# Kernel tuning notes

Measured on AMD Instinct MI355X. Metric: run time of the kernel, lower is better.

The kernel has to match this reference:

```python
import jax, jax.numpy as jnp
import numpy as np

N_NODES = 50000
N_EDGES = 800000
N_GRAPHS = 128
D_IN, D_HID, D_OUT = 128, 128, 128  # gnn_input_dim, gnn_hidden_dim, gnn_output_dim
EPS = 1e-5
NEG_SLOPE = 0.01


def setup_inputs() -> dict:
    key = jax.random.key(0)
    ks = jax.random.split(key, 16)
    x = jax.random.normal(ks[0], (N_NODES, D_IN), jnp.float32)
    edge_index = jax.random.randint(ks[1], (2, N_EDGES), 0, N_NODES, dtype=jnp.int64)
    batch = jnp.sort(jax.random.randint(ks[2], (N_NODES,), 0, N_GRAPHS, dtype=jnp.int64))

    def lin(k, fi, fo):
        return jax.random.normal(k, (fi, fo), jnp.float32) * (1.0 / np.sqrt(fi))

    d2, d4 = 2 * D_HID, 4 * D_HID
    return {
        "x": x, "edge_index": edge_index, "batch": batch, "batch_size": N_GRAPHS,
        "W1": lin(ks[3], D_IN, d2), "b1": jnp.zeros((d2,), jnp.float32),
        "g1": jnp.ones((d2,), jnp.float32), "be1": jnp.zeros((d2,), jnp.float32),
        "W2": lin(ks[4], d2, d4), "b2": jnp.zeros((d4,), jnp.float32),
        "g2": jnp.ones((d4,), jnp.float32), "be2": jnp.zeros((d4,), jnp.float32),
        "W3": lin(ks[5], d4, d4), "b3": jnp.zeros((d4,), jnp.float32),
        "g3": jnp.ones((d4,), jnp.float32), "be3": jnp.zeros((d4,), jnp.float32),
        "Wf": lin(ks[6], d4, D_OUT), "bf": jnp.zeros((D_OUT,), jnp.float32),
    }


def _layernorm(h, g, b):
    mu = jnp.mean(h, axis=-1, keepdims=True)
    var = jnp.mean(jnp.square(h - mu), axis=-1, keepdims=True)
    return (h - mu) * jax.lax.rsqrt(var + EPS) * g + b


def _gcn_conv(h, W, b, src, dst, norm, n):
    # h' = D^-1/2 (A+I) D^-1/2 (h W) + b   (PyG GCNConv with self-loops)
    m = h @ W                                    # [N, F_out]
    msg = m[src] * norm[:, None]                 # [E+N, F_out]
    return jax.ops.segment_sum(msg, dst, num_segments=n) + b


def reference(x, edge_index, batch, batch_size, W1, b1, g1, be1,
              W2, b2, g2, be2, W3, b3, g3, be3, Wf, bf):
    n = x.shape[0]
    loop = jnp.arange(n, dtype=edge_index.dtype)
    src = jnp.concatenate([edge_index[0], loop])
    dst = jnp.concatenate([edge_index[1], loop])
    deg = jax.ops.segment_sum(jnp.ones_like(dst, dtype=x.dtype), dst, num_segments=n)
    dinv = jax.lax.rsqrt(deg)                    # deg >= 1 due to self loops
    norm = dinv[src] * dinv[dst]

    h = _gcn_conv(x, W1, b1, src, dst, norm, n)
    h = jax.nn.leaky_relu(_layernorm(h, g1, be1), NEG_SLOPE)
    h = _gcn_conv(h, W2, b2, src, dst, norm, n)
    h = jax.nn.leaky_relu(_layernorm(h, g2, be2), NEG_SLOPE)
    h = _gcn_conv(h, W3, b3, src, dst, norm, n)
    h = _layernorm(h, g3, be3)

    # global average pool per graph
    sums = jax.ops.segment_sum(h, batch, num_segments=batch_size)
    cnt = jax.ops.segment_sum(jnp.ones((n,), h.dtype), batch, num_segments=batch_size)
    pooled = sums / jnp.maximum(cnt, 1.0)[:, None]
    return pooled @ Wf + bf
```

## Files before the change

### kernel.cpp

```cpp
#include <hip/hip_runtime.h>
#include <hip/hip_bf16.h>
#include <math.h>

#define GRAPHS 128
#define SCAN_B 256
#define BM 128
#define BN 128
#define PCH 128

typedef __attribute__((ext_vector_type(4))) int i32x4;

__device__ inline unsigned short f2b(float f) {
    unsigned int u = __float_as_uint(f);
    unsigned int r = (u + 0x7fffu + ((u >> 16) & 1u)) >> 16;
    return (unsigned short)r;
}
__device__ inline float b2f(unsigned short u) {
    return __uint_as_float(((unsigned int)u) << 16);
}
__device__ inline void unpack8(float* v, uint4 u) {
    v[0] = b2f(u.x & 0xffffu); v[1] = b2f(u.x >> 16);
    v[2] = b2f(u.y & 0xffffu); v[3] = b2f(u.y >> 16);
    v[4] = b2f(u.z & 0xffffu); v[5] = b2f(u.z >> 16);
    v[6] = b2f(u.w & 0xffffu); v[7] = b2f(u.w >> 16);
}

__device__ inline void gload16(const void* g, void* l) {
    typedef unsigned int __attribute__((address_space(1))) gu32;
    typedef unsigned int __attribute__((address_space(3))) su32;
    __builtin_amdgcn_global_load_lds((const gu32*)g, (su32*)l, 16, 0, 0);
}

__device__ inline int xcd_vid(int p, int nwg) {
    int q = nwg >> 3, r = nwg & 7, x = p & 7, ix = p >> 3;
    return (x < r ? x * (q + 1) : r * (q + 1) + (x - r) * q) + ix;
}


__global__ void k_count(const int* __restrict__ dst, int* __restrict__ cnt, int E) {
    int i = blockIdx.x * blockDim.x + threadIdx.x;
    if (i < E) atomicAdd(&cnt[dst[i]], 1);
}

__global__ void k_scan1(const int* __restrict__ cnt, int* __restrict__ excl,
                        int* __restrict__ bsum, int n) {
    __shared__ int sh[SCAN_B];
    int t = threadIdx.x;
    int i = blockIdx.x * SCAN_B + t;
    int v = (i < n) ? cnt[i] : 0;
    sh[t] = v;
    __syncthreads();
    for (int off = 1; off < SCAN_B; off <<= 1) {
        int x = (t >= off) ? sh[t - off] : 0;
        __syncthreads();
        sh[t] += x;
        __syncthreads();
    }
    if (i < n) excl[i] = sh[t] - v;
    if (t == SCAN_B - 1) bsum[blockIdx.x] = sh[t];
}

__global__ void k_scan2(int* __restrict__ bsum, int nb) {
    __shared__ int sh[SCAN_B];
    int t = threadIdx.x;
    int v = (t < nb) ? bsum[t] : 0;
    sh[t] = v;
    __syncthreads();
    for (int off = 1; off < SCAN_B; off <<= 1) {
        int x = (t >= off) ? sh[t - off] : 0;
        __syncthreads();
        sh[t] += x;
        __syncthreads();
    }
    if (t < nb) bsum[t] = sh[t] - v;
}

__global__ void k_scan3(int* __restrict__ rowstart, const int* __restrict__ bsum,
                        const int* __restrict__ cnt, float* __restrict__ dinv,
                        int* __restrict__ cursor, int n, int E) {
    int i = blockIdx.x * SCAN_B + threadIdx.x;
    if (i < n) {
        rowstart[i] += bsum[blockIdx.x];
        cursor[i] = 0;
        dinv[i] = rsqrtf((float)cnt[i] + 1.0f);
    }
    if (i == 0) rowstart[n] = E;
}

__global__ void k_scatter_csr(const int* __restrict__ src, const int* __restrict__ dst,
                              const float* __restrict__ dinv, const int* __restrict__ rowstart,
                              int* __restrict__ cursor, int2* __restrict__ csr, int E) {
    int e = blockIdx.x * blockDim.x + threadIdx.x;
    if (e >= E) return;
    int s = src[e], d = dst[e];
    int pos = rowstart[d] + atomicAdd(&cursor[d], 1);
    int2 c;
    c.x = s;
    c.y = __float_as_int(dinv[s] * dinv[d]);
    csr[pos] = c;
}


__global__ void k_wtq(const float* __restrict__ W1, const float* __restrict__ W2,
                      const float* __restrict__ W3, signed char* __restrict__ T1,
                      signed char* __restrict__ T2, signed char* __restrict__ T3,
                      float* __restrict__ S1, float* __restrict__ S2,
                      float* __restrict__ S3) {
    int w = blockIdx.x * 4 + (threadIdx.x >> 6);
    int lane = threadIdx.x & 63;
    const float* W; signed char* T; float* S; int K, N, col;
    if (w < 256) { W = W1; T = T1; S = S1; K = 128; N = 256; col = w; }
    else if (w < 768) { W = W2; T = T2; S = S2; K = 256; N = 512; col = w - 256; }
    else { W = W3; T = T3; S = S3; K = 512; N = 512; col = w - 768; }
    int epl = K >> 6;
    float v[8];
    float mx = 0.f;
    for (int j = 0; j < epl; ++j) {
        float x = W[(size_t)(lane * epl + j) * N + col];
        v[j] = x;
        mx = fmaxf(mx, fabsf(x));
    }
#pragma unroll
    for (int m = 1; m < 64; m <<= 1) mx = fmaxf(mx, __shfl_xor(mx, m));
    float inv = (mx > 0.f) ? 127.0f / mx : 0.f;
    signed char* tp = T + (size_t)col * K + lane * epl;
    for (int j = 0; j < epl; ++j) tp[j] = (signed char)__float2int_rn(v[j] * inv);
    if (lane == 0) S[col] = mx * (1.0f / 127.0f);
}


__global__ void k_x2q(const float* __restrict__ x, signed char* __restrict__ q,
                      float* __restrict__ sc, int n, int mpad) {
    int row = blockIdx.x * 4 + (threadIdx.x >> 6);
    int lane = threadIdx.x & 63;
    if (row >= mpad) return;
    signed char* qp = q + (size_t)row * 128 + lane * 2;
    if (row >= n) {
        *(unsigned short*)qp = 0;
        if (lane == 0) sc[row] = 0.f;
        return;
    }
    float2 v = *(const float2*)(x + (size_t)row * 128 + lane * 2);
    float mx = fmaxf(fabsf(v.x), fabsf(v.y));
#pragma unroll
    for (int m = 1; m < 64; m <<= 1) mx = fmaxf(mx, __shfl_xor(mx, m));
    float inv = (mx > 0.f) ? 127.0f / mx : 0.f;
    int q0 = __float2int_rn(v.x * inv), q1 = __float2int_rn(v.y * inv);
    *(unsigned short*)qp = (unsigned short)((q0 & 0xff) | ((q1 & 0xff) << 8));
    if (lane == 0) sc[row] = mx * (1.0f / 127.0f);
}


__device__ inline void acc8i(float* a, uint2 u, float w) {
    a[0] += (float)(signed char)(u.x) * w;
    a[1] += (float)(signed char)(u.x >> 8) * w;
    a[2] += (float)(signed char)(u.x >> 16) * w;
    a[3] += (float)(signed char)(u.x >> 24) * w;
    a[4] += (float)(signed char)(u.y) * w;
    a[5] += (float)(signed char)(u.y >> 8) * w;
    a[6] += (float)(signed char)(u.y >> 16) * w;
    a[7] += (float)(signed char)(u.y >> 24) * w;
}

template <int F>
__global__ void k_agg8(const signed char* __restrict__ q8, const float* __restrict__ scale,
                       signed char* __restrict__ qa, float* __restrict__ sa,
                       const int* __restrict__ rowstart, const int2* __restrict__ csr,
                       const float* __restrict__ dinv, int n, int mpad) {
    constexpr int TPN = F / 8;
    constexpr int NPB = 256 / TPN;
    int node = blockIdx.x * NPB + (int)(threadIdx.x / TPN);
    int sub = (int)(threadIdx.x % TPN);
    int fo = sub * 8;
    if (node >= mpad) return;
    signed char* outp = qa + (size_t)node * F + fo;
    if (node >= n) {
        *(uint2*)outp = uint2{0u, 0u};
        if (sub == 0) sa[node] = 0.f;
        return;
    }

    const signed char* qf = q8 + fo;
    float di = dinv[node];
    float a[8] = {};
    {
        uint2 u = *(const uint2*)(qf + (size_t)node * F);
        acc8i(a, u, di * di * scale[node]);
    }
    int b = rowstart[node], e = rowstart[node + 1];
    int j = b;
    for (; j + 2 <= e; j += 2) {
        int2 c0 = csr[j], c1 = csr[j + 1];
        uint2 u0 = *(const uint2*)(qf + (size_t)c0.x * F);
        uint2 u1 = *(const uint2*)(qf + (size_t)c1.x * F);
        float w0 = __int_as_float(c0.y) * scale[c0.x];
        float w1 = __int_as_float(c1.y) * scale[c1.x];
        acc8i(a, u0, w0);
        acc8i(a, u1, w1);
    }
    for (; j < e; ++j) {
        int2 c = csr[j];
        uint2 u = *(const uint2*)(qf + (size_t)c.x * F);
        acc8i(a, u, __int_as_float(c.y) * scale[c.x]);
    }
    float mx = 0.f;
#pragma unroll
    for (int k = 0; k < 8; ++k) mx = fmaxf(mx, fabsf(a[k]));
#pragma unroll
    for (int m = 1; m < TPN; m <<= 1) mx = fmaxf(mx, __shfl_xor(mx, m));
    float inv = (mx > 0.f) ? 127.0f / mx : 0.f;
    unsigned int o0 = 0, o1 = 0;
#pragma unroll
    for (int k = 0; k < 4; ++k) {
        o0 |= ((unsigned)(__float2int_rn(a[k] * inv) & 0xff)) << (8 * k);
        o1 |= ((unsigned)(__float2int_rn(a[k + 4] * inv) & 0xff)) << (8 * k);
    }
    *(uint2*)outp = uint2{o0, o1};
    if (sub == 0) sa[node] = mx * (1.0f / 127.0f);
}


__global__ __launch_bounds__(256) void k_gemm_i8(
    const signed char* __restrict__ A, const float* __restrict__ srow,
    const signed char* __restrict__ BT, const float* __restrict__ scol,
    const float* __restrict__ bias, unsigned short* __restrict__ C,
    int K, int N, int ncb) {
    __shared__ __align__(16) char sA[BM * 128];
    __shared__ __align__(16) char sB[BN * 128];

    const int vid = xcd_vid((int)blockIdx.x, (int)gridDim.x);
    const int rb = vid / ncb;
    const int cb = vid - rb * ncb;
    const int tid = threadIdx.x;
    const int lane = tid & 63;
    const int wave = tid >> 6;
    const int wr = wave >> 1, wc = wave & 1;
    const size_t row0 = (size_t)rb * BM;
    const size_t col0 = (size_t)cb * BN;

    const signed char* srcA[4];
    const signed char* srcB[4];
    char* dstA[4];
    char* dstB[4];
#pragma unroll
    for (int c = 0; c < 4; ++c) {
        int idx = c * 256 + tid;
        int row = idx >> 3;
        int cbl = ((idx & 7) << 4) ^ ((row & 7) << 4);
        srcA[c] = A + (row0 + row) * K + cbl;
        srcB[c] = BT + (col0 + row) * K + cbl;
        dstA[c] = sA + idx * 16;
        dstB[c] = sB + idx * 16;
    }

    const int fr = lane & 15;
    const int fg = lane >> 4;
    const int fsw = (lane & 7) << 4;
    int offA[4][2], offB[4][2];
#pragma unroll
    for (int t = 0; t < 4; ++t)
#pragma unroll
        for (int kk = 0; kk < 2; ++kk) {
            offA[t][kk] = (wr * 64 + t * 16 + fr) * 128 + ((kk * 64 + fg * 16) ^ fsw);
            offB[t][kk] = (wc * 64 + t * 16 + fr) * 128 + ((kk * 64 + fg * 16) ^ fsw);
        }

    i32x4 acc[4][4] = {};

    for (int k0 = 0; k0 < K; k0 += 128) {
#pragma unroll
        for (int c = 0; c < 4; ++c) gload16(srcA[c] + k0, dstA[c]);
#pragma unroll
        for (int c = 0; c < 4; ++c) gload16(srcB[c] + k0, dstB[c]);
        __syncthreads();
#pragma unroll
        for (int kk = 0; kk < 2; ++kk) {
            i32x4 av[4], bv[4];
#pragma unroll
            for (int t = 0; t < 4; ++t) av[t] = *(const i32x4*)(sA + offA[t][kk]);
#pragma unroll
            for (int t = 0; t < 4; ++t) bv[t] = *(const i32x4*)(sB + offB[t][kk]);
#pragma unroll
            for (int i = 0; i < 4; ++i)
#pragma unroll
                for (int j = 0; j < 4; ++j)
                    acc[i][j] = __builtin_amdgcn_mfma_i32_16x16x64_i8(av[i], bv[j],
                                                                      acc[i][j], 0, 0, 0);
        }
        __syncthreads();
    }

    float sr[4][4];
#pragma unroll
    for (int i = 0; i < 4; ++i)
#pragma unroll
        for (int q = 0; q < 4; ++q)
            sr[i][q] = srow[row0 + wr * 64 + i * 16 + fg * 4 + q];

#pragma unroll
    for (int i = 0; i < 4; ++i) {
#pragma unroll
        for (int j = 0; j < 4; ++j) {
            size_t r = row0 + wr * 64 + i * 16 + fg * 4;
            size_t cc = col0 + wc * 64 + j * 16 + fr;
            float scc = scol[cc];
            float bb = bias[cc];
#pragma unroll
            for (int q = 0; q < 4; ++q)
                C[(r + q) * N + cc] = f2b((float)acc[i][j][q] * (sr[i][q] * scc) + bb);
        }
    }
}


template <int F, bool LRELU>
__global__ void k_lnr8(const unsigned short* __restrict__ z, signed char* __restrict__ q8,
                       float* __restrict__ scale, const float* __restrict__ g,
                       const float* __restrict__ be, int mpad) {
    constexpr int V = F / 64;
    int row = blockIdx.x * 4 + (threadIdx.x >> 6);
    int lane = threadIdx.x & 63;
    const unsigned short* p = z + (size_t)row * F + lane * V;
    float v[V];
    if constexpr (V == 8) {
        uint4 u = *(const uint4*)p;
        unpack8(v, u);
    } else {
        uint2 u = *(const uint2*)p;
        v[0] = b2f(u.x & 0xffffu); v[1] = b2f(u.x >> 16);
        v[2] = b2f(u.y & 0xffffu); v[3] = b2f(u.y >> 16);
    }
    float s = 0.f, q = 0.f;
#pragma unroll
    for (int k = 0; k < V; ++k) { s += v[k]; q += v[k] * v[k]; }
#pragma unroll
    for (int m = 1; m < 64; m <<= 1) {
        s += __shfl_xor(s, m);
        q += __shfl_xor(q, m);
    }
    float mu = s * (1.0f / F);
    float var = q * (1.0f / F) - mu * mu;
    float rs = rsqrtf(var + 1e-5f);

    float y[V];
    float mx = 0.f;
#pragma unroll
    for (int k = 0; k < V; ++k) {
        float yy = (v[k] - mu) * rs * g[lane * V + k] + be[lane * V + k];
        if (LRELU) yy = fmaxf(yy, 0.f) + 0.01f * fminf(yy, 0.f);
        y[k] = yy;
        mx = fmaxf(mx, fabsf(yy));
    }
#pragma unroll
    for (int m = 1; m < 64; m <<= 1) mx = fmaxf(mx, __shfl_xor(mx, m));

    float inv = (mx > 0.f) ? 127.0f / mx : 0.f;
    unsigned int ob[V / 4];
#pragma unroll
    for (int k = 0; k < V; k += 4) {
        int q0 = __float2int_rn(y[k] * inv);
        int q1 = __float2int_rn(y[k + 1] * inv);
        int q2 = __float2int_rn(y[k + 2] * inv);
        int q3 = __float2int_rn(y[k + 3] * inv);
        ob[k / 4] = (q0 & 0xff) | ((q1 & 0xff) << 8) | ((q2 & 0xff) << 16) | ((q3 & 0xff) << 24);
    }
    signed char* qp = q8 + (size_t)row * F + lane * V;
    if constexpr (V == 8) *(uint2*)qp = *(uint2*)ob;
    else                  *(unsigned int*)qp = ob[0];
    if (lane == 0) scale[row] = mx * (1.0f / 127.0f);
}


__global__ void k_pool4(const unsigned short* __restrict__ z, const float* __restrict__ g,
                        const float* __restrict__ be, const int* __restrict__ batch,
                        float* __restrict__ pooled, int n) {
    int i0 = blockIdx.x * PCH;
    int iend = i0 + PCH; if (iend > n) iend = n;
    int w = threadIdx.x >> 6, lane = threadIdx.x & 63;
    int f0 = lane * 8;
    float gk[8], ek[8];
    {
        float4 ga = *(const float4*)(g + f0), gb = *(const float4*)(g + f0 + 4);
        float4 ea = *(const float4*)(be + f0), eb = *(const float4*)(be + f0 + 4);
        gk[0] = ga.x; gk[1] = ga.y; gk[2] = ga.z; gk[3] = ga.w;
        gk[4] = gb.x; gk[5] = gb.y; gk[6] = gb.z; gk[7] = gb.w;
        ek[0] = ea.x; ek[1] = ea.y; ek[2] = ea.z; ek[3] = ea.w;
        ek[4] = eb.x; ek[5] = eb.y; ek[6] = eb.z; ek[7] = eb.w;
    }
    float a[8] = {};
    int cur = -1;
    for (int i = i0 + w; i < iend; i += 4) {
        int gg = batch[i];
        if (gg != cur) {
            if (cur >= 0) {
                float* pp = pooled + (size_t)cur * 512 + f0;
#pragma unroll
                for (int k = 0; k < 8; ++k) atomicAdd(&pp[k], a[k]);
            }
#pragma unroll
            for (int k = 0; k < 8; ++k) a[k] = 0.f;
            cur = gg;
        }
        uint4 u = *(const uint4*)(z + (size_t)i * 512 + f0);
        float v[8]; unpack8(v, u);
        float s = 0.f, q = 0.f;
#pragma unroll
        for (int k = 0; k < 8; ++k) { s += v[k]; q += v[k] * v[k]; }
#pragma unroll
        for (int m = 1; m < 64; m <<= 1) {
            s += __shfl_xor(s, m);
            q += __shfl_xor(q, m);
        }
        float mu = s * (1.0f / 512.0f);
        float var = q * (1.0f / 512.0f) - mu * mu;
        float rs = rsqrtf(var + 1e-5f);
#pragma unroll
        for (int k = 0; k < 8; ++k) a[k] += (v[k] - mu) * rs * gk[k] + ek[k];
    }
    if (cur >= 0) {
        float* pp = pooled + (size_t)cur * 512 + f0;
#pragma unroll
        for (int k = 0; k < 8; ++k) atomicAdd(&pp[k], a[k]);
    }
}


__global__ void k_final(const float* __restrict__ pooled, const int* __restrict__ batch,
                        const float* __restrict__ Wf, const float* __restrict__ bf,
                        float* __restrict__ out, int n) {
    int gph = blockIdx.x;
    int o = threadIdx.x;
    int lo = 0, hi = n;
    while (lo < hi) { int mid = (lo + hi) >> 1; if (batch[mid] < gph) lo = mid + 1; else hi = mid; }
    int start = lo;
    lo = start; hi = n;
    while (lo < hi) { int mid = (lo + hi) >> 1; if (batch[mid] < gph + 1) lo = mid + 1; else hi = mid; }
    int end = lo;
    float inv = 1.0f / fmaxf((float)(end - start), 1.0f);

    __shared__ float p[512];
    for (int k = threadIdx.x; k < 512; k += 128) p[k] = pooled[(size_t)gph * 512 + k] * inv;
    __syncthreads();
    float acc = bf[o];
#pragma unroll 8
    for (int k = 0; k < 512; ++k) acc += p[k] * Wf[(size_t)k * 128 + o];
    out[(size_t)gph * 128 + o] = acc;
}


static inline size_t align_up(size_t x) { return (x + 255) & ~(size_t)255; }

extern "C" void kernel_launch(void* const* d_in, const int* in_sizes, int n_in,
                              void* d_out, int out_size, void* d_ws, size_t ws_size,
                              hipStream_t stream) {
    const float* x     = (const float*)d_in[0];
    const int*   ei    = (const int*)d_in[1];
    const int*   batch = (const int*)d_in[2];
    const float* W1 = (const float*)d_in[4],  *b1 = (const float*)d_in[5];
    const float* g1 = (const float*)d_in[6],  *be1= (const float*)d_in[7];
    const float* W2 = (const float*)d_in[8],  *b2 = (const float*)d_in[9];
    const float* g2 = (const float*)d_in[10], *be2= (const float*)d_in[11];
    const float* W3 = (const float*)d_in[12], *b3 = (const float*)d_in[13];
    const float* g3 = (const float*)d_in[14], *be3= (const float*)d_in[15];
    const float* Wf = (const float*)d_in[16], *bf = (const float*)d_in[17];
    float* out = (float*)d_out;

    const int N = in_sizes[0] / 128;
    const int E = in_sizes[1] / 2;
    const int Mpad = ((N + BM - 1) / BM) * BM;
    const int* src = ei;
    const int* dst = ei + E;

    char* ws = (char*)d_ws;
    size_t off = 0;
    auto take = [&](size_t bytes) { char* p = ws + off; off += align_up(bytes); return p; };

    unsigned short* zb      = (unsigned short*)take((size_t)Mpad * 512 * 2);
    signed char*    qa      = (signed char*)take((size_t)Mpad * 512);
    float*          sa      = (float*)take((size_t)Mpad * 4);
    signed char*    q8      = (signed char*)take((size_t)Mpad * 512);
    float*          scale   = (float*)take((size_t)Mpad * 4);
    signed char*    q8x     = (signed char*)take((size_t)Mpad * 128);
    float*          sx      = (float*)take((size_t)Mpad * 4);
    signed char*    wq1     = (signed char*)take((size_t)256 * 128);
    signed char*    wq2     = (signed char*)take((size_t)512 * 256);
    signed char*    wq3     = (signed char*)take((size_t)512 * 512);
    float*          sc1     = (float*)take(256 * 4);
    float*          sc2     = (float*)take(512 * 4);
    float*          sc3     = (float*)take(512 * 4);
    float*          dinv    = (float*)take((size_t)N * 4);
    int*            rowstart= (int*)  take((size_t)(N + 1) * 4);
    int*            cnt     = (int*)  take((size_t)N * 4);
    int*            cursor  = (int*)  take((size_t)N * 4);
    int*            bsum    = (int*)  take((size_t)SCAN_B * 4);
    int2*           csr     = (int2*) take((size_t)E * 8);
    float*          pooled  = (float*)take((size_t)GRAPHS * 512 * 4);

    const int nb = (N + SCAN_B - 1) / SCAN_B;
    const int NR4 = Mpad / 4;

    hipMemsetAsync(cnt, 0, (size_t)N * 4, stream);
    k_count<<<(E + 255) / 256, 256, 0, stream>>>(dst, cnt, E);
    k_scan1<<<nb, SCAN_B, 0, stream>>>(cnt, rowstart, bsum, N);
    k_scan2<<<1, SCAN_B, 0, stream>>>(bsum, nb);
    k_scan3<<<nb, SCAN_B, 0, stream>>>(rowstart, bsum, cnt, dinv, cursor, N, E);
    k_scatter_csr<<<(E + 255) / 256, 256, 0, stream>>>(src, dst, dinv, rowstart, cursor, csr, E);

    k_wtq<<<320, 256, 0, stream>>>(W1, W2, W3, wq1, wq2, wq3, sc1, sc2, sc3);

    k_x2q<<<NR4, 256, 0, stream>>>(x, q8x, sx, N, Mpad);

    k_agg8<128><<<Mpad / 16, 256, 0, stream>>>(q8x, sx, qa, sa, rowstart, csr, dinv, N, Mpad);
    k_gemm_i8<<<(Mpad / BM) * 2, 256, 0, stream>>>(qa, sa, wq1, sc1, b1, zb, 128, 256, 2);
    k_lnr8<256, true><<<NR4, 256, 0, stream>>>(zb, q8, scale, g1, be1, Mpad);

    k_agg8<256><<<Mpad / 8, 256, 0, stream>>>(q8, scale, qa, sa, rowstart, csr, dinv, N, Mpad);
    k_gemm_i8<<<(Mpad / BM) * 4, 256, 0, stream>>>(qa, sa, wq2, sc2, b2, zb, 256, 512, 4);
    k_lnr8<512, true><<<NR4, 256, 0, stream>>>(zb, q8, scale, g2, be2, Mpad);

    k_agg8<512><<<Mpad / 4, 256, 0, stream>>>(q8, scale, qa, sa, rowstart, csr, dinv, N, Mpad);
    k_gemm_i8<<<(Mpad / BM) * 4, 256, 0, stream>>>(qa, sa, wq3, sc3, b3, zb, 512, 512, 4);

    hipMemsetAsync(pooled, 0, (size_t)GRAPHS * 512 * 4, stream);
    k_pool4<<<(N + PCH - 1) / PCH, 256, 0, stream>>>(zb, g3, be3, batch, pooled, N);
    k_final<<<GRAPHS, 128, 0, stream>>>(pooled, batch, Wf, bf, out, N);
}
```

Measured before the change: 412.1 us.

## Use integer fixed-point accumulation in aggregation, widen per-thread loads, fuse prep kernels

The SpMM aggregation now quantizes each edge weight to a fixed-point integer (scaled by 2^21) and accumulates int8 features with 24-bit integer multiplies into int32 accumulators instead of float FMAs. Each thread now handles 16 bytes per gather, so half as many threads do the work. The weight quantization and input quantization kernels are merged into one launch. This cuts ALU and conversion work and launch overhead, but risks int32 overflow or precision loss from weight rounding on high-degree nodes.

```diff
diff --git a/kernel.cpp b/kernel.cpp
--- a/kernel.cpp
+++ b/kernel.cpp
@@ -7,6 +7,7 @@
 #define BM 128
 #define BN 128
 #define PCH 128
+#define WSCALE 2097152.0f
 
 typedef __attribute__((ext_vector_type(4))) int i32x4;
 
@@ -101,43 +102,42 @@
 }
 
 
-__global__ void k_wtq(const float* __restrict__ W1, const float* __restrict__ W2,
-                      const float* __restrict__ W3, signed char* __restrict__ T1,
-                      signed char* __restrict__ T2, signed char* __restrict__ T3,
-                      float* __restrict__ S1, float* __restrict__ S2,
-                      float* __restrict__ S3) {
-    int w = blockIdx.x * 4 + (threadIdx.x >> 6);
+__global__ void k_prep(const float* __restrict__ W1, const float* __restrict__ W2,
+                       const float* __restrict__ W3, signed char* __restrict__ T1,
+                       signed char* __restrict__ T2, signed char* __restrict__ T3,
+                       float* __restrict__ S1, float* __restrict__ S2,
+                       float* __restrict__ S3, const float* __restrict__ x,
+                       signed char* __restrict__ qx, float* __restrict__ sx,
+                       int n, int mpad) {
     int lane = threadIdx.x & 63;
-    const float* W; signed char* T; float* S; int K, N, col;
-    if (w < 256) { W = W1; T = T1; S = S1; K = 128; N = 256; col = w; }
-    else if (w < 768) { W = W2; T = T2; S = S2; K = 256; N = 512; col = w - 256; }
-    else { W = W3; T = T3; S = S3; K = 512; N = 512; col = w - 768; }
-    int epl = K >> 6;
-    float v[8];
-    float mx = 0.f;
-    for (int j = 0; j < epl; ++j) {
-        float x = W[(size_t)(lane * epl + j) * N + col];
-        v[j] = x;
-        mx = fmaxf(mx, fabsf(x));
-    }
-#pragma unroll
-    for (int m = 1; m < 64; m <<= 1) mx = fmaxf(mx, __shfl_xor(mx, m));
-    float inv = (mx > 0.f) ? 127.0f / mx : 0.f;
-    signed char* tp = T + (size_t)col * K + lane * epl;
-    for (int j = 0; j < epl; ++j) tp[j] = (signed char)__float2int_rn(v[j] * inv);
-    if (lane == 0) S[col] = mx * (1.0f / 127.0f);
-}
-
-
-__global__ void k_x2q(const float* __restrict__ x, signed char* __restrict__ q,
-                      float* __restrict__ sc, int n, int mpad) {
-    int row = blockIdx.x * 4 + (threadIdx.x >> 6);
-    int lane = threadIdx.x & 63;
+    if (blockIdx.x < 320) {
+        int w = blockIdx.x * 4 + (threadIdx.x >> 6);
+        const float* W; signed char* T; float* S; int K, N, col;
+        if (w < 256) { W = W1; T = T1; S = S1; K = 128; N = 256; col = w; }
+        else if (w < 768) { W = W2; T = T2; S = S2; K = 256; N = 512; col = w - 256; }
+        else { W = W3; T = T3; S = S3; K = 512; N = 512; col = w - 768; }
+        int epl = K >> 6;
+        float v[8];
+        float mx = 0.f;
+        for (int j = 0; j < epl; ++j) {
+            float xx = W[(size_t)(lane * epl + j) * N + col];
+            v[j] = xx;
+            mx = fmaxf(mx, fabsf(xx));
+        }
+#pragma unroll
+        for (int m = 1; m < 64; m <<= 1) mx = fmaxf(mx, __shfl_xor(mx, m));
+        float inv = (mx > 0.f) ? 127.0f / mx : 0.f;
+        signed char* tp = T + (size_t)col * K + lane * epl;
+        for (int j = 0; j < epl; ++j) tp[j] = (signed char)__float2int_rn(v[j] * inv);
+        if (lane == 0) S[col] = mx * (1.0f / 127.0f);
+        return;
+    }
+    int row = (blockIdx.x - 320) * 4 + (threadIdx.x >> 6);
     if (row >= mpad) return;
-    signed char* qp = q + (size_t)row * 128 + lane * 2;
+    signed char* qp = qx + (size_t)row * 128 + lane * 2;
     if (row >= n) {
         *(unsigned short*)qp = 0;
-        if (lane == 0) sc[row] = 0.f;
+        if (lane == 0) sx[row] = 0.f;
         return;
     }
     float2 v = *(const float2*)(x + (size_t)row * 128 + lane * 2);
@@ -147,19 +147,21 @@
     float inv = (mx > 0.f) ? 127.0f / mx : 0.f;
     int q0 = __float2int_rn(v.x * inv), q1 = __float2int_rn(v.y * inv);
     *(unsigned short*)qp = (unsigned short)((q0 & 0xff) | ((q1 & 0xff) << 8));
-    if (lane == 0) sc[row] = mx * (1.0f / 127.0f);
-}
-
-
-__device__ inline void acc8i(float* a, uint2 u, float w) {
-    a[0] += (float)(signed char)(u.x) * w;
-    a[1] += (float)(signed char)(u.x >> 8) * w;
-    a[2] += (float)(signed char)(u.x >> 16) * w;
-    a[3] += (float)(signed char)(u.x >> 24) * w;
-    a[4] += (float)(signed char)(u.y) * w;
-    a[5] += (float)(signed char)(u.y >> 8) * w;
-    a[6] += (float)(signed char)(u.y >> 16) * w;
-    a[7] += (float)(signed char)(u.y >> 24) * w;
+    if (lane == 0) sx[row] = mx * (1.0f / 127.0f);
+}
+
+
+__device__ inline void accw(int* a, unsigned int u, int wq) {
+    a[0] += __mul24((int)(signed char)(u), wq);
+    a[1] += __mul24((int)(signed char)(u >> 8), wq);
+    a[2] += __mul24((int)(signed char)(u >> 16), wq);
+    a[3] += __mul24((int)(signed char)(u >> 24), wq);
+}
+__device__ inline void acc16(int* a, uint4 u, int wq) {
+    accw(a, u.x, wq);
+    accw(a + 4, u.y, wq);
+    accw(a + 8, u.z, wq);
+    accw(a + 12, u.w, wq);
 }
 
 template <int F>
@@ -167,56 +169,63 @@
                        signed char* __restrict__ qa, float* __restrict__ sa,
                        const int* __restrict__ rowstart, const int2* __restrict__ csr,
                        const float* __restrict__ dinv, int n, int mpad) {
-    constexpr int TPN = F / 8;
+    constexpr int TPN = F / 16;
     constexpr int NPB = 256 / TPN;
     int node = blockIdx.x * NPB + (int)(threadIdx.x / TPN);
     int sub = (int)(threadIdx.x % TPN);
-    int fo = sub * 8;
+    int fo = sub * 16;
     if (node >= mpad) return;
     signed char* outp = qa + (size_t)node * F + fo;
     if (node >= n) {
-        *(uint2*)outp = uint2{0u, 0u};
+        uint4 z = {0u, 0u, 0u, 0u};
+        *(uint4*)outp = z;
         if (sub == 0) sa[node] = 0.f;
         return;
     }
 
     const signed char* qf = q8 + fo;
     float di = dinv[node];
-    float a[8] = {};
+    int a[16] = {};
     {
-        uint2 u = *(const uint2*)(qf + (size_t)node * F);
-        acc8i(a, u, di * di * scale[node]);
+        uint4 u = *(const uint4*)(qf + (size_t)node * F);
+        int wq = __float2int_rn(di * di * scale[node] * WSCALE);
+        acc16(a, u, wq);
     }
     int b = rowstart[node], e = rowstart[node + 1];
     int j = b;
     for (; j + 2 <= e; j += 2) {
         int2 c0 = csr[j], c1 = csr[j + 1];
-        uint2 u0 = *(const uint2*)(qf + (size_t)c0.x * F);
-        uint2 u1 = *(const uint2*)(qf + (size_t)c1.x * F);
-        float w0 = __int_as_float(c0.y) * scale[c0.x];
-        float w1 = __int_as_float(c1.y) * scale[c1.x];
-        acc8i(a, u0, w0);
-        acc8i(a, u1, w1);
+        uint4 u0 = *(const uint4*)(qf + (size_t)c0.x * F);
+        uint4 u1 = *(const uint4*)(qf + (size_t)c1.x * F);
+        int w0 = __float2int_rn(__int_as_float(c0.y) * scale[c0.x] * WSCALE);
+        int w1 = __float2int_rn(__int_as_float(c1.y) * scale[c1.x] * WSCALE);
+        acc16(a, u0, w0);
+        acc16(a, u1, w1);
     }
     for (; j < e; ++j) {
         int2 c = csr[j];
-        uint2 u = *(const uint2*)(qf + (size_t)c.x * F);
-        acc8i(a, u, __int_as_float(c.y) * scale[c.x]);
-    }
-    float mx = 0.f;
-#pragma unroll
-    for (int k = 0; k < 8; ++k) mx = fmaxf(mx, fabsf(a[k]));
-#pragma unroll
-    for (int m = 1; m < TPN; m <<= 1) mx = fmaxf(mx, __shfl_xor(mx, m));
-    float inv = (mx > 0.f) ? 127.0f / mx : 0.f;
-    unsigned int o0 = 0, o1 = 0;
-#pragma unroll
-    for (int k = 0; k < 4; ++k) {
-        o0 |= ((unsigned)(__float2int_rn(a[k] * inv) & 0xff)) << (8 * k);
-        o1 |= ((unsigned)(__float2int_rn(a[k + 4] * inv) & 0xff)) << (8 * k);
-    }
-    *(uint2*)outp = uint2{o0, o1};
-    if (sub == 0) sa[node] = mx * (1.0f / 127.0f);
+        uint4 u = *(const uint4*)(qf + (size_t)c.x * F);
+        int wq = __float2int_rn(__int_as_float(c.y) * scale[c.x] * WSCALE);
+        acc16(a, u, wq);
+    }
+    int amax = 0;
+#pragma unroll
+    for (int k = 0; k < 16; ++k) amax = max(amax, abs(a[k]));
+#pragma unroll
+    for (int m = 1; m < TPN; m <<= 1) amax = max(amax, __shfl_xor(amax, m));
+
+    float inv = (amax > 0) ? 127.0f / (float)amax : 0.f;
+    unsigned int ob[4];
+#pragma unroll
+    for (int wi = 0; wi < 4; ++wi) {
+        unsigned int o = 0;
+#pragma unroll
+        for (int k = 0; k < 4; ++k)
+            o |= ((unsigned)(__float2int_rn((float)a[wi * 4 + k] * inv) & 0xff)) << (8 * k);
+        ob[wi] = o;
+    }
+    *(uint4*)outp = *(uint4*)ob;
+    if (sub == 0) sa[node] = (float)amax * (1.0f / (127.0f * WSCALE));
 }
 
 
@@ -506,19 +515,18 @@
     k_scan3<<<nb, SCAN_B, 0, stream>>>(rowstart, bsum, cnt, dinv, cursor, N, E);
     k_scatter_csr<<<(E + 255) / 256, 256, 0, stream>>>(src, dst, dinv, rowstart, cursor, csr, E);
 
-    k_wtq<<<320, 256, 0, stream>>>(W1, W2, W3, wq1, wq2, wq3, sc1, sc2, sc3);
-
-    k_x2q<<<NR4, 256, 0, stream>>>(x, q8x, sx, N, Mpad);
-
-    k_agg8<128><<<Mpad / 16, 256, 0, stream>>>(q8x, sx, qa, sa, rowstart, csr, dinv, N, Mpad);
+    k_prep<<<320 + NR4, 256, 0, stream>>>(W1, W2, W3, wq1, wq2, wq3, sc1, sc2, sc3,
+                                          x, q8x, sx, N, Mpad);
+
+    k_agg8<128><<<Mpad / 32, 256, 0, stream>>>(q8x, sx, qa, sa, rowstart, csr, dinv, N, Mpad);
     k_gemm_i8<<<(Mpad / BM) * 2, 256, 0, stream>>>(qa, sa, wq1, sc1, b1, zb, 128, 256, 2);
     k_lnr8<256, true><<<NR4, 256, 0, stream>>>(zb, q8, scale, g1, be1, Mpad);
 
-    k_agg8<256><<<Mpad / 8, 256, 0, stream>>>(q8, scale, qa, sa, rowstart, csr, dinv, N, Mpad);
+    k_agg8<256><<<Mpad / 16, 256, 0, stream>>>(q8, scale, qa, sa, rowstart, csr, dinv, N, Mpad);
     k_gemm_i8<<<(Mpad / BM) * 4, 256, 0, stream>>>(qa, sa, wq2, sc2, b2, zb, 256, 512, 4);
     k_lnr8<512, true><<<NR4, 256, 0, stream>>>(zb, q8, scale, g2, be2, Mpad);
 
-    k_agg8<512><<<Mpad / 4, 256, 0, stream>>>(q8, scale, qa, sa, rowstart, csr, dinv, N, Mpad);
+    k_agg8<512><<<Mpad / 8, 256, 0, stream>>>(q8, scale, qa, sa, rowstart, csr, dinv, N, Mpad);
     k_gemm_i8<<<(Mpad / BM) * 4, 256, 0, stream>>>(qa, sa, wq3, sc3, b3, zb, 512, 512, 4);
 
     hipMemsetAsync(pooled, 0, (size_t)GRAPHS * 512 * 4, stream);
```

Measured after the change: 394.1 us. 1.05x faster.
